# Kernel tuning notes

Hardware: AMD Instinct MI355X
Metric: run time of the kernel (lower is better)

## Reference

```python
import jax, jax.numpy as jnp
import numpy as np

HEADS = 16
LN_EPS = 1e-5


def setup_inputs() -> dict:
    key = jax.random.key(0)
    ks = jax.random.split(key, 8)
    B, S, D = 2, 2048, 1024
    F = 4 * D
    std = 0.02
    return {
        "x": jax.random.normal(ks[0], (B, S, D), jnp.float32),
        # QKV projections (stored as (in, out)); kaiming-normal-like scale
        "Wq": jax.random.normal(ks[1], (D, D), jnp.float32) * std,
        "bq": jnp.zeros((D,), jnp.float32),
        "Wk": jax.random.normal(ks[2], (D, D), jnp.float32) * std,
        "bk": jnp.zeros((D,), jnp.float32),
        "Wv": jax.random.normal(ks[3], (D, D), jnp.float32) * std,
        "bv": jnp.zeros((D,), jnp.float32),
        # FFN
        "W1": jax.random.normal(ks[4], (D, F), jnp.float32) * std,
        "b1": jnp.zeros((F,), jnp.float32),
        "W2": jax.random.normal(ks[5], (F, D), jnp.float32) * std,
        "b2": jnp.zeros((D,), jnp.float32),
        # LayerNorm
        "gamma": jnp.ones((D,), jnp.float32),
        "beta": jnp.zeros((D,), jnp.float32),
    }


def reference(x, Wq, bq, Wk, bk, Wv, bv, W1, b1, W2, b2, gamma, beta):
    B, S, D = x.shape
    H = HEADS
    hd = D // H
    # QKV projections -> [B, H, S, hd]
    Q = (x @ Wq + bq).reshape(B, S, H, hd).transpose(0, 2, 1, 3)
    K = (x @ Wk + bk).reshape(B, S, H, hd).transpose(0, 2, 1, 3)
    V = (x @ Wv + bv).reshape(B, S, H, hd).transpose(0, 2, 1, 3)
    # scores scaled by sqrt(embedding_dim), faithful to source (not head_dim)
    scores = jnp.einsum('bhqd,bhkd->bhqk', Q, K) / jnp.sqrt(jnp.asarray(D, x.dtype))
    attn = jax.nn.softmax(scores, axis=-1)
    # diagonal_training: zero the diagonal of the post-softmax attention matrix
    attn = attn * (1.0 - jnp.eye(S, dtype=attn.dtype))
    out = jnp.einsum('bhqk,bhkd->bhqd', attn, V)
    out = out.transpose(0, 2, 1, 3).reshape(B, S, D)
    # dropout is identity in eval mode
    h = jax.nn.gelu(out @ W1 + b1, approximate=False) @ W2 + b2
    # LayerNorm
    mu = jnp.mean(h, axis=-1, keepdims=True)
    var = jnp.var(h, axis=-1, keepdims=True)
    return (h - mu) * jax.lax.rsqrt(var + LN_EPS) * gamma + beta
```

## Files before the change

kernel.cpp:

```cpp
#include <hip/hip_runtime.h>

using bf16x8 = __attribute__((ext_vector_type(8))) short;
using f32x4  = __attribute__((ext_vector_type(4))) float;

__device__ __forceinline__ float b2f(ushort u) {
  union { unsigned int i; float f; } v; v.i = ((unsigned int)u) << 16; return v.f;
}
__device__ __forceinline__ ushort f2b(float f) {
  unsigned int x = __float_as_uint(f);
  unsigned int r = (x + 0x7FFFu + ((x >> 16) & 1u)) >> 16;
  return (ushort)r;
}
__device__ __forceinline__ unsigned cvt_pk_bf16(float a, float b) {
  unsigned r;
  asm("v_cvt_pk_bf16_f32 %0, %1, %2" : "=v"(r) : "v"(a), "v"(b));
  return r;
}

__device__ __forceinline__ void gld_lds16(const void* g, void* l) {
  __builtin_amdgcn_global_load_lds(
      (const __attribute__((address_space(1))) void*)g,
      (__attribute__((address_space(3))) void*)l, 16, 0, 0);
}


__global__ void cast_bf16_kernel(const float* __restrict__ in, ushort* __restrict__ out, int n) {
  int i = (blockIdx.x * blockDim.x + threadIdx.x) * 4;
  if (i < n) {
    float4 v = *(const float4*)(in + i);
    ushort4 o = make_ushort4(f2b(v.x), f2b(v.y), f2b(v.z), f2b(v.w));
    *(ushort4*)(out + i) = o;
  }
}

__global__ void transpose_cast_kernel(const float* __restrict__ in, ushort* __restrict__ out,
                                      int R, int C) {
  __shared__ float tile[32][33];
  int tx = threadIdx.x, ty = threadIdx.y;
  int cb = blockIdx.x * 32, rb = blockIdx.y * 32;
  for (int i = ty; i < 32; i += 8)
    tile[i][tx] = in[(size_t)(rb + i) * C + (cb + tx)];
  __syncthreads();
  for (int i = ty; i < 32; i += 8)
    out[(size_t)(cb + i) * R + (rb + tx)] = f2b(tile[tx][i]);
}

__global__ void transpose_v_kernel(const ushort* __restrict__ V, ushort* __restrict__ Vt) {
  __shared__ ushort t[32][33];
  int bh = blockIdx.z;
  int s0 = blockIdx.x * 32, d0 = blockIdx.y * 32;
  const ushort* Vb = V + (size_t)bh * 2048 * 64;
  ushort* Vtb = Vt + (size_t)bh * 64 * 2048;
  int tx = threadIdx.x, ty = threadIdx.y;
  for (int i = ty; i < 32; i += 8) t[i][tx] = Vb[(size_t)(s0 + i) * 64 + d0 + tx];
  __syncthreads();
  for (int i = ty; i < 32; i += 8) Vtb[(size_t)(d0 + i) * 2048 + s0 + tx] = t[tx][i];
}


#define BM 128
#define BN 128
#define BK 32

template<int EPI>
__global__ __launch_bounds__(256) void gemm_bf16(
    const ushort* __restrict__ A, const ushort* __restrict__ Bt,
    const float* __restrict__ bias, void* __restrict__ Cout, void* __restrict__ Cout2,
    int M, int N, int Kstride, int k_len)
{
  __shared__ ushort Asm_[2][BM * BK];
  __shared__ ushort Bsm_[2][BN * BK];
  const int bm = blockIdx.x * BM, bn = blockIdx.y * BN;
  const int k_begin = blockIdx.z * k_len;
  const int tid = threadIdx.x;
  const int lane = tid & 63, w = tid >> 6;
  const int wm = (w >> 1) * 64, wn = (w & 1) * 64;
  const int g = lane >> 4, c = lane & 15;
  const int srow = tid >> 2, scol = (tid & 3) * 8;
  const int soff = srow * 32 + scol;

  const ushort* gA0 = A  + (size_t)(bm + srow) * Kstride + k_begin + scol;
  const ushort* gA1 = gA0 + (size_t)64 * Kstride;
  const ushort* gB0 = Bt + (size_t)(bn + srow) * Kstride + k_begin + scol;
  const ushort* gB1 = gB0 + (size_t)64 * Kstride;

  f32x4 acc[4][4] = {};
  const int nt = k_len / BK;

  gld_lds16(gA0, &Asm_[0][soff]);
  gld_lds16(gA1, &Asm_[0][64 * 32 + soff]);
  gld_lds16(gB0, &Bsm_[0][soff]);
  gld_lds16(gB1, &Bsm_[0][64 * 32 + soff]);
  __syncthreads();

  int cur = 0;
  for (int t = 0; t < nt; ++t) {
    if (t + 1 < nt) {
      int k0 = (t + 1) * BK;
      gld_lds16(gA0 + k0, &Asm_[cur ^ 1][soff]);
      gld_lds16(gA1 + k0, &Asm_[cur ^ 1][64 * 32 + soff]);
      gld_lds16(gB0 + k0, &Bsm_[cur ^ 1][soff]);
      gld_lds16(gB1 + k0, &Bsm_[cur ^ 1][64 * 32 + soff]);
    }
    bf16x8 af[4], bfr[4];
    #pragma unroll
    for (int m = 0; m < 4; ++m)
      af[m] = *(const bf16x8*)&Asm_[cur][(wm + m * 16 + c) * 32 + g * 8];
    #pragma unroll
    for (int n = 0; n < 4; ++n)
      bfr[n] = *(const bf16x8*)&Bsm_[cur][(wn + n * 16 + c) * 32 + g * 8];
    #pragma unroll
    for (int m = 0; m < 4; ++m)
      #pragma unroll
      for (int n = 0; n < 4; ++n)
        acc[m][n] = __builtin_amdgcn_mfma_f32_16x16x32_bf16(af[m], bfr[n], acc[m][n], 0, 0, 0);
    __syncthreads();
    cur ^= 1;
  }

  #pragma unroll
  for (int n = 0; n < 4; ++n) {
    int col = bn + wn + n * 16 + c;
    float bia = bias ? bias[col] : 0.0f;
    #pragma unroll
    for (int m = 0; m < 4; ++m) {
      #pragma unroll
      for (int r = 0; r < 4; ++r) {
        int row = bm + wm + m * 16 + g * 4 + r;
        float v = acc[m][n][r] + bia;
        if (EPI == 1) {
          float u = 0.7978845608028654f * (v + 0.044715f * v * v * v);
          float au = fabsf(u);
          float e = __expf(-2.0f * au);
          float th = (1.0f - e) / (1.0f + e);
          th = copysignf(th, u);
          v = 0.5f * v * (1.0f + th);
        }
        if (EPI == 2) {
          float* dst = (blockIdx.z == 0) ? (float*)Cout : (float*)Cout2;
          dst[(size_t)row * N + col] = v;
        } else if (EPI == 3) {
          int b = row >> 11, s = row & 2047;
          int which = col >> 10, cc = col & 1023;
          int hh = cc >> 6, d = cc & 63;
          ((ushort*)Cout)[(size_t)which * 4194304 +
                          ((size_t)((b * 16 + hh) * 2048 + s)) * 64 + d] = f2b(v);
        } else {
          ((ushort*)Cout)[(size_t)row * N + col] = f2b(v);
        }
      }
    }
  }
}


#define ATT_SC2 0.0450842202f

__global__ __launch_bounds__(512) void attn_kernel(
    const ushort* __restrict__ Q, const ushort* __restrict__ K,
    const ushort* __restrict__ V, const ushort* __restrict__ Vt,
    ushort* __restrict__ Out)
{
  const int bh = blockIdx.y;
  const int b = bh >> 4, h = bh & 15;
  const int q0 = blockIdx.x * 128;
  const int tid = threadIdx.x;
  const int w = tid >> 6, lane = tid & 63;
  const int hi = lane >> 4, c = lane & 15;
  const int qw = q0 + w * 16;

  const ushort* Qb = Q + (size_t)bh * 2048 * 64;
  const ushort* Kb = K + (size_t)bh * 2048 * 64;
  const ushort* Vb = V + (size_t)bh * 2048 * 64;
  const ushort* Vtb = Vt + (size_t)bh * 64 * 2048;

  __shared__ ushort Ksm[2][64 * 64];
  __shared__ ushort Vsm[2][64 * 64];
  __shared__ ushort Psm[8][16 * 72];

  const int srow = tid >> 3;
  const int sslot = tid & 7;
  const int scolx = ((sslot ^ (srow & 7)) * 8);
  const ushort* gK = Kb + (size_t)srow * 64 + scolx;
  const ushort* gV = Vtb + (size_t)srow * 2048 + scolx;

  bf16x8 qf0 = *(const bf16x8*)(Qb + (size_t)(qw + c) * 64 + hi * 8);
  bf16x8 qf1 = *(const bf16x8*)(Qb + (size_t)(qw + c) * 64 + 32 + hi * 8);

  f32x4 acc[4] = {};
  float m_run = -1e30f, l_run = 0.f;

  gld_lds16(gK, &Ksm[0][tid * 8]);
  gld_lds16(gV, &Vsm[0][tid * 8]);
  __syncthreads();

  const int nt = 2048 / 64;
  for (int t = 0; t < nt; ++t) {
    const int buf = t & 1;
    if (t + 1 < nt) {
      gld_lds16(gK + (size_t)(t + 1) * 64 * 64, &Ksm[buf ^ 1][tid * 8]);
      gld_lds16(gV + (size_t)(t + 1) * 64,      &Vsm[buf ^ 1][tid * 8]);
    }

    f32x4 sv[4];
    #pragma unroll
    for (int sub = 0; sub < 4; ++sub) {
      int rr = sub * 16 + c;
      int sw = (rr & 7) * 8;
      bf16x8 k0 = *(const bf16x8*)&Ksm[buf][rr * 64 + ((hi * 8) ^ sw)];
      bf16x8 k1 = *(const bf16x8*)&Ksm[buf][rr * 64 + ((32 + hi * 8) ^ sw)];
      f32x4 z = {};
      __builtin_amdgcn_s_setprio(1);
      z = __builtin_amdgcn_mfma_f32_16x16x32_bf16(k0, qf0, z, 0, 0, 0);
      z = __builtin_amdgcn_mfma_f32_16x16x32_bf16(k1, qf1, z, 0, 0, 0);
      __builtin_amdgcn_s_setprio(0);
      #pragma unroll
      for (int r = 0; r < 4; ++r) sv[sub][r] = z[r] * ATT_SC2;
    }

    float tm = -1e30f;
    #pragma unroll
    for (int sub = 0; sub < 4; ++sub)
      #pragma unroll
      for (int r = 0; r < 4; ++r) tm = fmaxf(tm, sv[sub][r]);
    tm = fmaxf(tm, __shfl_xor(tm, 16));
    tm = fmaxf(tm, __shfl_xor(tm, 32));
    float mnew = fmaxf(m_run, tm);
    float p[16];
    float psum = 0.f;
    #pragma unroll
    for (int sub = 0; sub < 4; ++sub)
      #pragma unroll
      for (int r = 0; r < 4; ++r) { float e = exp2f(sv[sub][r] - mnew); p[sub * 4 + r] = e; psum += e; }
    psum += __shfl_xor(psum, 16);
    psum += __shfl_xor(psum, 32);
    float f = exp2f(m_run - mnew);
    l_run = l_run * f + psum;
    m_run = mnew;

    #pragma unroll
    for (int r = 0; r < 4; ++r) {
      float fr = __shfl(f, hi * 4 + r, 16);
      #pragma unroll
      for (int dsub = 0; dsub < 4; ++dsub) acc[dsub][r] *= fr;
    }

    #pragma unroll
    for (int sub = 0; sub < 4; ++sub) {
      uint2 pk;
      pk.x = cvt_pk_bf16(p[sub * 4 + 0], p[sub * 4 + 1]);
      pk.y = cvt_pk_bf16(p[sub * 4 + 2], p[sub * 4 + 3]);
      *(uint2*)&Psm[w][c * 72 + sub * 16 + hi * 4] = pk;
    }
    asm volatile("" ::: "memory");

    bf16x8 pa0 = *(const bf16x8*)&Psm[w][c * 72 + hi * 8];
    bf16x8 pa1 = *(const bf16x8*)&Psm[w][c * 72 + 32 + hi * 8];
    __builtin_amdgcn_s_setprio(1);
    #pragma unroll
    for (int dsub = 0; dsub < 4; ++dsub) {
      int rr = dsub * 16 + c;
      int sw = (rr & 7) * 8;
      bf16x8 v0 = *(const bf16x8*)&Vsm[buf][rr * 64 + ((hi * 8) ^ sw)];
      bf16x8 v1 = *(const bf16x8*)&Vsm[buf][rr * 64 + ((32 + hi * 8) ^ sw)];
      acc[dsub] = __builtin_amdgcn_mfma_f32_16x16x32_bf16(pa0, v0, acc[dsub], 0, 0, 0);
      acc[dsub] = __builtin_amdgcn_mfma_f32_16x16x32_bf16(pa1, v1, acc[dsub], 0, 0, 0);
    }
    __builtin_amdgcn_s_setprio(0);

    __syncthreads();
  }

  #pragma unroll
  for (int r = 0; r < 4; ++r) {
    int q = qw + hi * 4 + r;
    float part = 0.f;
    #pragma unroll
    for (int t = 0; t < 4; ++t)
      part += b2f(Qb[(size_t)q * 64 + c * 4 + t]) * b2f(Kb[(size_t)q * 64 + c * 4 + t]);
    #pragma unroll
    for (int off = 1; off < 16; off <<= 1) part += __shfl_xor(part, off);
    float mq = __shfl(m_run, hi * 4 + r, 16);
    float lq = __shfl(l_run, hi * 4 + r, 16);
    float pqq = exp2f(part * ATT_SC2 - mq);
    float inv = 1.f / lq;
    #pragma unroll
    for (int dsub = 0; dsub < 4; ++dsub) {
      float vq = b2f(Vb[(size_t)q * 64 + dsub * 16 + c]);
      float o = (acc[dsub][r] - pqq * vq) * inv;
      Out[((size_t)(b * 2048 + q) * 16 + h) * 64 + dsub * 16 + c] = f2b(o);
    }
  }
}


__global__ __launch_bounds__(256) void ln_kernel(float* __restrict__ h,
                                                 const float* __restrict__ p1,
                                                 const float* __restrict__ b2,
                                                 const float* __restrict__ gamma,
                                                 const float* __restrict__ beta) {
  int row = blockIdx.x, tid = threadIdx.x;
  float* hr = h + (size_t)row * 1024;
  const float* pr = p1 + (size_t)row * 1024;
  float4 v = ((const float4*)hr)[tid];
  float4 p = ((const float4*)pr)[tid];
  float4 bb = ((const float4*)b2)[tid];
  v.x += p.x + bb.x; v.y += p.y + bb.y; v.z += p.z + bb.z; v.w += p.w + bb.w;
  float s = v.x + v.y + v.z + v.w;
  #pragma unroll
  for (int off = 1; off < 64; off <<= 1) s += __shfl_xor(s, off);
  __shared__ float red[2][4];
  int wv = tid >> 6, lane = tid & 63;
  if (lane == 0) red[0][wv] = s;
  __syncthreads();
  float mu = (red[0][0] + red[0][1] + red[0][2] + red[0][3]) * (1.0f / 1024.0f);
  float dx = v.x - mu, dy = v.y - mu, dz = v.z - mu, dw = v.w - mu;
  float q = dx * dx + dy * dy + dz * dz + dw * dw;
  #pragma unroll
  for (int off = 1; off < 64; off <<= 1) q += __shfl_xor(q, off);
  if (lane == 0) red[1][wv] = q;
  __syncthreads();
  float var = (red[1][0] + red[1][1] + red[1][2] + red[1][3]) * (1.0f / 1024.0f);
  float is = rsqrtf(var + 1e-5f);
  float4 gm = ((const float4*)gamma)[tid];
  float4 bt = ((const float4*)beta)[tid];
  float4 o;
  o.x = dx * is * gm.x + bt.x;
  o.y = dy * is * gm.y + bt.y;
  o.z = dz * is * gm.z + bt.z;
  o.w = dw * is * gm.w + bt.w;
  ((float4*)hr)[tid] = o;
}


extern "C" void kernel_launch(void* const* d_in, const int* in_sizes, int n_in,
                              void* d_out, int out_size, void* d_ws, size_t ws_size,
                              hipStream_t stream) {
  const float* x  = (const float*)d_in[0];
  const float* Wq = (const float*)d_in[1];
  const float* bq = (const float*)d_in[2];
  const float* Wk = (const float*)d_in[3];
  const float* bk = (const float*)d_in[4];
  const float* Wv = (const float*)d_in[5];
  const float* bv = (const float*)d_in[6];
  const float* W1 = (const float*)d_in[7];
  const float* b1 = (const float*)d_in[8];
  const float* W2 = (const float*)d_in[9];
  const float* b2 = (const float*)d_in[10];
  const float* gamma = (const float*)d_in[11];
  const float* beta  = (const float*)d_in[12];
  float* out = (float*)d_out;

  char* ws = (char*)d_ws;
  const size_t MB = 1u << 20;
  ushort* xb    = (ushort*)(ws + 0);
  ushort* Wqkvt = (ushort*)(ws + 8 * MB);
  ushort* Qb    = (ushort*)(ws + 14 * MB);
  ushort* Kb    = (ushort*)(ws + 22 * MB);
  ushort* Vb    = (ushort*)(ws + 30 * MB);
  ushort* Vt    = (ushort*)(ws + 38 * MB);
  ushort* AO    = (ushort*)(ws + 46 * MB);
  ushort* W1t   = (ushort*)(ws + 0);
  ushort* h1    = (ushort*)(ws + 14 * MB);
  ushort* W2t   = (ushort*)(ws + 46 * MB);
  float*  p1    = (float*)(ws + 0);
  float*  bqkv  = (float*)(ws + 61 * MB);

  (void)hipMemcpyAsync(bqkv,        bq, 4096, hipMemcpyDeviceToDevice, stream);
  (void)hipMemcpyAsync(bqkv + 1024, bk, 4096, hipMemcpyDeviceToDevice, stream);
  (void)hipMemcpyAsync(bqkv + 2048, bv, 4096, hipMemcpyDeviceToDevice, stream);

  dim3 tb(32, 8);
  cast_bf16_kernel<<<4096, 256, 0, stream>>>(x, xb, 4194304);
  transpose_cast_kernel<<<dim3(32, 32), tb, 0, stream>>>(Wq, Wqkvt, 1024, 1024);
  transpose_cast_kernel<<<dim3(32, 32), tb, 0, stream>>>(Wk, Wqkvt + 1024 * 1024, 1024, 1024);
  transpose_cast_kernel<<<dim3(32, 32), tb, 0, stream>>>(Wv, Wqkvt + 2 * 1024 * 1024, 1024, 1024);

  gemm_bf16<3><<<dim3(32, 24), 256, 0, stream>>>(xb, Wqkvt, bqkv, Qb, nullptr,
                                                 4096, 3072, 1024, 1024);

  transpose_cast_kernel<<<dim3(128, 32), tb, 0, stream>>>(W1, W1t, 1024, 4096);
  transpose_v_kernel<<<dim3(64, 2, 32), tb, 0, stream>>>(Vb, Vt);

  attn_kernel<<<dim3(16, 32), 512, 0, stream>>>(Qb, Kb, Vb, Vt, AO);

  gemm_bf16<1><<<dim3(32, 32), 256, 0, stream>>>(AO, W1t, b1, h1, nullptr,
                                                 4096, 4096, 1024, 1024);
  transpose_cast_kernel<<<dim3(32, 128), tb, 0, stream>>>(W2, W2t, 4096, 1024);
  gemm_bf16<2><<<dim3(32, 8, 2), 256, 0, stream>>>(h1, W2t, nullptr, out, p1,
                                                   4096, 1024, 4096, 2048);

  ln_kernel<<<4096, 256, 0, stream>>>(out, p1, b2, gamma, beta);
}
```

Baseline: 270.5 us.

## Add 256x256 triple-buffered GEMM kernel for QKV and FFN1 projections

Adds a 512-thread GEMM with 256x256 output tiles, a three-stage LDS ring fed by direct global-to-LDS loads, XOR-swizzled LDS layout, and grid swizzling across 8 groups for L2 locality. MFMA phases are interleaved with issuing the next stage's loads, using explicit waitcnt, sched_barrier and setprio. The QKV and W1 GEMMs now use it instead of the 128x128 double-buffered kernel, aiming for more data reuse per tile and better overlap of memory with compute. The cost is 96KB of dynamic LDS and a large register footprint, so occupancy drops, and only 192 or 256 workgroups are launched for the 256-CU device.

```diff
diff --git a/kernel.cpp b/kernel.cpp
--- a/kernel.cpp
+++ b/kernel.cpp
@@ -55,6 +55,129 @@
   for (int i = ty; i < 32; i += 8) t[i][tx] = Vb[(size_t)(s0 + i) * 64 + d0 + tx];
   __syncthreads();
   for (int i = ty; i < 32; i += 8) Vtb[(size_t)(d0 + i) * 2048 + s0 + tx] = t[tx][i];
+}
+
+
+template<int EPI>
+__global__ __launch_bounds__(512) void gemm256(
+    const ushort* __restrict__ A, const ushort* __restrict__ Bt,
+    const float* __restrict__ bias, void* __restrict__ Cout,
+    int M, int N, int K)
+{
+  extern __shared__ ushort lds[];
+
+  const int nwg = gridDim.x * gridDim.y;
+  const int bid = blockIdx.y * gridDim.x + blockIdx.x;
+  const int cpx = nwg >> 3;
+  const int swz = (bid & 7) * cpx + (bid >> 3);
+  const int bm = (swz % gridDim.x) * 256;
+  const int bn = (swz / gridDim.x) * 256;
+
+  const int tid = threadIdx.x;
+  const int lane = tid & 63, w = tid >> 6;
+  const int wr = w >> 2, wc = w & 3;
+  const int g = lane >> 4, c = lane & 15;
+  const int swz8 = ((g ^ (c & 3)) * 8);
+
+  const int srow = tid >> 2;
+  const int scol = (((tid & 3) ^ (srow & 3)) * 8);
+  const ushort* gA = A  + (size_t)(bm + srow) * K + scol;
+  const ushort* gB = Bt + (size_t)(bn + srow) * K + scol;
+  const size_t rowK128 = (size_t)128 * K;
+
+  const int NT = K / 32;
+  f32x4 acc[8][4] = {};
+
+  #pragma unroll
+  for (int kt = 0; kt < 2; ++kt) {
+    ushort* sA = &lds[kt * 16384];
+    gld_lds16(gA + (size_t)kt * 32,            sA + tid * 8);
+    gld_lds16(gA + rowK128 + (size_t)kt * 32,  sA + 4096 + tid * 8);
+    gld_lds16(gB + (size_t)kt * 32,            sA + 8192 + tid * 8);
+    gld_lds16(gB + rowK128 + (size_t)kt * 32,  sA + 8192 + 4096 + tid * 8);
+  }
+
+  for (int kt = 0; kt < NT; ++kt) {
+    ushort* sA = &lds[(kt % 3) * 16384];
+    ushort* sB = sA + 8192;
+    const int stage_kt = kt + 2;
+    ushort* sS = &lds[(stage_kt % 3) * 16384];
+
+    __builtin_amdgcn_sched_barrier(0);
+    if (kt + 1 < NT) asm volatile("s_waitcnt vmcnt(4)" ::: "memory");
+    else             asm volatile("s_waitcnt vmcnt(0)" ::: "memory");
+    __builtin_amdgcn_s_barrier();
+    __builtin_amdgcn_sched_barrier(0);
+
+    bf16x8 bf[4], af[4];
+    #pragma unroll
+    for (int n = 0; n < 4; ++n)
+      bf[n] = *(const bf16x8*)&sB[(wc * 64 + n * 16 + c) * 32 + swz8];
+    #pragma unroll
+    for (int m = 0; m < 4; ++m)
+      af[m] = *(const bf16x8*)&sA[(wr * 128 + m * 16 + c) * 32 + swz8];
+    if (stage_kt < NT) {
+      gld_lds16(gA + (size_t)stage_kt * 32,           sS + tid * 8);
+      gld_lds16(gA + rowK128 + (size_t)stage_kt * 32, sS + 4096 + tid * 8);
+    }
+    asm volatile("s_waitcnt lgkmcnt(0)" ::: "memory");
+    __builtin_amdgcn_sched_barrier(0);
+    __builtin_amdgcn_s_setprio(1);
+    #pragma unroll
+    for (int m = 0; m < 4; ++m)
+      #pragma unroll
+      for (int n = 0; n < 4; ++n)
+        acc[m][n] = __builtin_amdgcn_mfma_f32_16x16x32_bf16(af[m], bf[n], acc[m][n], 0, 0, 0);
+    __builtin_amdgcn_s_setprio(0);
+    __builtin_amdgcn_sched_barrier(0);
+
+    #pragma unroll
+    for (int m = 0; m < 4; ++m)
+      af[m] = *(const bf16x8*)&sA[(wr * 128 + 64 + m * 16 + c) * 32 + swz8];
+    if (stage_kt < NT) {
+      gld_lds16(gB + (size_t)stage_kt * 32,           sS + 8192 + tid * 8);
+      gld_lds16(gB + rowK128 + (size_t)stage_kt * 32, sS + 8192 + 4096 + tid * 8);
+    }
+    asm volatile("s_waitcnt lgkmcnt(0)" ::: "memory");
+    __builtin_amdgcn_sched_barrier(0);
+    __builtin_amdgcn_s_setprio(1);
+    #pragma unroll
+    for (int m = 0; m < 4; ++m)
+      #pragma unroll
+      for (int n = 0; n < 4; ++n)
+        acc[4 + m][n] = __builtin_amdgcn_mfma_f32_16x16x32_bf16(af[m], bf[n], acc[4 + m][n], 0, 0, 0);
+    __builtin_amdgcn_s_setprio(0);
+    __builtin_amdgcn_sched_barrier(0);
+  }
+
+  #pragma unroll
+  for (int n = 0; n < 4; ++n) {
+    int col = bn + wc * 64 + n * 16 + c;
+    float bia = bias[col];
+    #pragma unroll
+    for (int mf = 0; mf < 8; ++mf) {
+      #pragma unroll
+      for (int r = 0; r < 4; ++r) {
+        int row = bm + wr * 128 + mf * 16 + g * 4 + r;
+        float v = acc[mf][n][r] + bia;
+        if (EPI == 1) {
+          float u = 0.7978845608028654f * (v + 0.044715f * v * v * v);
+          float au = fabsf(u);
+          float e = __expf(-2.0f * au);
+          float th = (1.0f - e) / (1.0f + e);
+          th = copysignf(th, u);
+          v = 0.5f * v * (1.0f + th);
+          ((ushort*)Cout)[(size_t)row * N + col] = f2b(v);
+        } else {
+          int b = row >> 11, s = row & 2047;
+          int which = col >> 10, cc = col & 1023;
+          int hh = cc >> 6, d = cc & 63;
+          ((ushort*)Cout)[(size_t)which * 4194304 +
+                          ((size_t)((b * 16 + hh) * 2048 + s)) * 64 + d] = f2b(v);
+        }
+      }
+    }
+  }
 }
 
 
@@ -128,23 +251,9 @@
       for (int r = 0; r < 4; ++r) {
         int row = bm + wm + m * 16 + g * 4 + r;
         float v = acc[m][n][r] + bia;
-        if (EPI == 1) {
-          float u = 0.7978845608028654f * (v + 0.044715f * v * v * v);
-          float au = fabsf(u);
-          float e = __expf(-2.0f * au);
-          float th = (1.0f - e) / (1.0f + e);
-          th = copysignf(th, u);
-          v = 0.5f * v * (1.0f + th);
-        }
         if (EPI == 2) {
           float* dst = (blockIdx.z == 0) ? (float*)Cout : (float*)Cout2;
           dst[(size_t)row * N + col] = v;
-        } else if (EPI == 3) {
-          int b = row >> 11, s = row & 2047;
-          int which = col >> 10, cc = col & 1023;
-          int hh = cc >> 6, d = cc & 63;
-          ((ushort*)Cout)[(size_t)which * 4194304 +
-                          ((size_t)((b * 16 + hh) * 2048 + s)) * 64 + d] = f2b(v);
         } else {
           ((ushort*)Cout)[(size_t)row * N + col] = f2b(v);
         }
@@ -376,16 +485,15 @@
   transpose_cast_kernel<<<dim3(32, 32), tb, 0, stream>>>(Wk, Wqkvt + 1024 * 1024, 1024, 1024);
   transpose_cast_kernel<<<dim3(32, 32), tb, 0, stream>>>(Wv, Wqkvt + 2 * 1024 * 1024, 1024, 1024);
 
-  gemm_bf16<3><<<dim3(32, 24), 256, 0, stream>>>(xb, Wqkvt, bqkv, Qb, nullptr,
-                                                 4096, 3072, 1024, 1024);
+  gemm256<3><<<dim3(16, 12), 512, 98304, stream>>>(xb, Wqkvt, bqkv, Qb, 4096, 3072, 1024);
 
   transpose_cast_kernel<<<dim3(128, 32), tb, 0, stream>>>(W1, W1t, 1024, 4096);
   transpose_v_kernel<<<dim3(64, 2, 32), tb, 0, stream>>>(Vb, Vt);
 
   attn_kernel<<<dim3(16, 32), 512, 0, stream>>>(Qb, Kb, Vb, Vt, AO);
 
-  gemm_bf16<1><<<dim3(32, 32), 256, 0, stream>>>(AO, W1t, b1, h1, nullptr,
-                                                 4096, 4096, 1024, 1024);
+  gemm256<1><<<dim3(16, 16), 512, 98304, stream>>>(AO, W1t, b1, h1, 4096, 4096, 1024);
+
   transpose_cast_kernel<<<dim3(32, 128), tb, 0, stream>>>(W2, W2t, 4096, 1024);
   gemm_bf16<2><<<dim3(32, 8, 2), 256, 0, stream>>>(h1, W2t, nullptr, out, p1,
                                                    4096, 1024, 4096, 2048);
```

After: 264.6 us. 2.2% less time.
